# Kernel tuning notes

Hardware: AMD Instinct MI355X
Metric: run time of the kernel (lower is better)

## Reference

```python
import jax, jax.numpy as jnp
import numpy as np

B = 16384
QD = 2048   # query_dim
KD = 1024   # key_dim
HID = 1024  # hidden_dim = min(QD, KD)
NH = 16     # num_heads
HD = HID // NH  # head_dim = 64
LN_EPS = 1e-5


def _ln(x, w, b):
    m = jnp.mean(x, axis=-1, keepdims=True)
    v = jnp.mean((x - m) ** 2, axis=-1, keepdims=True)
    return (x - m) * jax.lax.rsqrt(v + LN_EPS) * w + b


def _lin(x, W, b):
    return x @ W.T + b


def setup_inputs() -> dict:
    key = jax.random.key(0)
    ks = jax.random.split(key, 12)
    p = lambda k, shape: jax.random.normal(k, shape, jnp.float32) * 0.02
    return dict(
        query_features=jax.random.normal(ks[0], (B, QD), jnp.float32),
        key_features=jax.random.normal(ks[1], (B, KD), jnp.float32),
        Wq=p(ks[2], (HID, QD)), bq=jnp.zeros((HID,), jnp.float32),
        ln_q_w=jnp.ones((HID,), jnp.float32), ln_q_b=jnp.zeros((HID,), jnp.float32),
        Wk=p(ks[3], (HID, KD)), bk=jnp.zeros((HID,), jnp.float32),
        ln_k_w=jnp.ones((HID,), jnp.float32), ln_k_b=jnp.zeros((HID,), jnp.float32),
        Wvq=p(ks[4], (HID, QD)), bvq=jnp.zeros((HID,), jnp.float32),
        Wvk=p(ks[5], (HID, KD)), bvk=jnp.zeros((HID,), jnp.float32),
        Wo=p(ks[6], (QD, HID)), bo=jnp.zeros((QD,), jnp.float32),
        ln_o_w=jnp.ones((QD,), jnp.float32), ln_o_b=jnp.zeros((QD,), jnp.float32),
        Wg1=p(ks[7], (HID, QD + KD)), bg1=jnp.zeros((HID,), jnp.float32),
        Wg2=p(ks[8], (1, HID)), bg2=jnp.zeros((1,), jnp.float32),
        Wc1=p(ks[9], (HID, QD + KD)), bc1=jnp.zeros((HID,), jnp.float32),
        Wc2=p(ks[10], (1, HID)), bc2=jnp.zeros((1,), jnp.float32),
    )


def reference(query_features, key_features,
              Wq, bq, ln_q_w, ln_q_b,
              Wk, bk, ln_k_w, ln_k_b,
              Wvq, bvq, Wvk, bvk,
              Wo, bo, ln_o_w, ln_o_b,
              Wg1, bg1, Wg2, bg2,
              Wc1, bc1, Wc2, bc2):
    b = query_features.shape[0]
    q = _ln(_lin(query_features, Wq, bq), ln_q_w, ln_q_b)      # [B, HID]
    k = _ln(_lin(key_features, Wk, bk), ln_k_w, ln_k_b)        # [B, HID]
    v_q = _lin(query_features, Wvq, bvq)  # computed in torch but unused
    v_k = _lin(key_features, Wvk, bvk)    # [B, HID]
    q = q.reshape(b, NH, HD)
    k = k.reshape(b, NH, HD)
    v_k = v_k.reshape(b, NH, HD)
    # NOTE: attention mixes over the HEAD axis (j == num_heads), per original einsum
    scores = jnp.einsum('bhd,bjd->bhj', q, k) / np.sqrt(HD).astype(np.float32)
    attn = jax.nn.softmax(scores, axis=-1)  # dropout p effectively 0 / eval mode
    attended = jnp.einsum('bhj,bjd->bhd', attn, v_k).reshape(b, HID)
    output = _ln(_lin(attended, Wo, bo), ln_o_w, ln_o_b)       # [B, QD]
    combined = jnp.concatenate([query_features, key_features], axis=1)  # [B, QD+KD]
    gate = jax.nn.sigmoid(_lin(jax.nn.gelu(_lin(combined, Wg1, bg1), approximate=False), Wg2, bg2))
    chem = jax.nn.sigmoid(_lin(jax.nn.gelu(_lin(combined, Wc1, bc1), approximate=False), Wc2, bc2))
    effective_gate = gate * chem  # [B, 1]
    return query_features + effective_gate * output
```

## Files before the change

kernel.cpp:

```cpp
#include <hip/hip_runtime.h>
#include <stdint.h>

#define QD 2048
#define KD 1024
#define HID 1024
#define NH 16
#define HD 64
#define CMBD 3072

typedef float  f32x4   __attribute__((ext_vector_type(4)));
typedef short  short8  __attribute__((ext_vector_type(8)));
typedef short  short4v __attribute__((ext_vector_type(4)));
typedef float  float4v __attribute__((ext_vector_type(4)));

__device__ inline float bf2f(short s) {
  unsigned u = ((unsigned)(unsigned short)s) << 16;
  return __builtin_bit_cast(float, u);
}
__device__ inline short f2bf(float f) {
  unsigned u = __builtin_bit_cast(unsigned, f);
  u = u + 0x7fff + ((u >> 16) & 1);
  return (short)(u >> 16);
}

__global__ void cvt_bf16(const float* __restrict__ s, short* __restrict__ d) {
  size_t i = ((size_t)blockIdx.x * blockDim.x + threadIdx.x) * 4;
  float4v v = *(const float4v*)(s + i);
  short4v o;
  o[0] = f2bf(v[0]); o[1] = f2bf(v[1]); o[2] = f2bf(v[2]); o[3] = f2bf(v[3]);
  *(short4v*)(d + i) = o;
}

__global__ void cvt_concat(const float* __restrict__ s, short* __restrict__ d,
                           int ncols4, int ldd) {
  int i = blockIdx.x * blockDim.x + threadIdx.x;
  int row = i / ncols4;
  int c4  = i - row * ncols4;
  float4v v = *(const float4v*)(s + (size_t)row * (ncols4 * 4) + c4 * 4);
  short4v o;
  o[0] = f2bf(v[0]); o[1] = f2bf(v[1]); o[2] = f2bf(v[2]); o[3] = f2bf(v[3]);
  *(short4v*)(d + (size_t)row * ldd + c4 * 4) = o;
}

#define EPI_NONE 0
#define EPI_GELU 1

typedef const __attribute__((address_space(1))) void gvoid_t;
typedef __attribute__((address_space(3))) void lvoid_t;

#define WAIT_VM(n)  asm volatile("s_waitcnt vmcnt(" #n ")" ::: "memory")

template<int EPI>
__global__ __launch_bounds__(512, 2)
void gemm256(const short* __restrict__ A, size_t lda,
             const short* __restrict__ W,
             const float* __restrict__ bias,
             short* __restrict__ C, int N, int K) {
  extern __shared__ short ls[];
  const int tid  = threadIdx.x;
  const int lane = tid & 63;
  const int wave = tid >> 6;
  const int wm = wave >> 2, wn = wave & 3;
  const int fr = lane & 15, kq4 = lane >> 4;

  const int nwg = gridDim.x * gridDim.y;
  const int lin = blockIdx.y * gridDim.x + blockIdx.x;
  const int cpx = nwg >> 3;
  const int nid = (lin & 7) * cpx + (lin >> 3);
  const int bx = nid % gridDim.x, by = nid / gridDim.x;
  const size_t rowBase = (size_t)by * 256;
  const size_t colBase = (size_t)bx * 256;

  const int NT = K >> 5;

  f32x4 acc[8][4];
#pragma unroll
  for (int mi = 0; mi < 8; mi++)
#pragma unroll
    for (int ni = 0; ni < 4; ni++) acc[mi][ni] = (f32x4){0.f, 0.f, 0.f, 0.f};

  const int frsw = (kq4 ^ ((fr >> 1) & 3)) * 8;
  const int aoff = (wm * 128 + fr) * 32 + frsw;
  const int boff = 8192 + (wn * 64 + fr) * 32 + frsw;

  const int grow  = tid >> 2;
  const int slotx = (tid & 3) ^ ((tid >> 3) & 3);
  const short* pA0 = A + (rowBase + grow) * lda + slotx * 8;
  const short* pA1 = pA0 + (size_t)128 * lda;
  const short* pB0 = W + (colBase + grow) * (size_t)K + slotx * 8;
  const short* pB1 = pB0 + (size_t)128 * K;
  short* const dst0 = ls + tid * 8;

  auto STAGE = [&](int slot) {
    short* d = dst0 + slot * 16384;
    __builtin_amdgcn_global_load_lds((gvoid_t*)pA0, (lvoid_t*)d,           16, 0, 0);
    __builtin_amdgcn_global_load_lds((gvoid_t*)pA1, (lvoid_t*)(d + 4096),  16, 0, 0);
    __builtin_amdgcn_global_load_lds((gvoid_t*)pB0, (lvoid_t*)(d + 8192),  16, 0, 0);
    __builtin_amdgcn_global_load_lds((gvoid_t*)pB1, (lvoid_t*)(d + 12288), 16, 0, 0);
    pA0 += 32; pA1 += 32; pB0 += 32; pB1 += 32;
  };

  STAGE(0); STAGE(1); STAGE(2);
  WAIT_VM(4);
  __builtin_amdgcn_s_barrier();

  short8 cf[12], nf[12];
  {
    const short* sl = ls;
#pragma unroll
    for (int m = 0; m < 8; m++) cf[m] = *(const short8*)(sl + aoff + m * 512);
#pragma unroll
    for (int n = 0; n < 4; n++) cf[8 + n] = *(const short8*)(sl + boff + n * 512);
  }

  for (int i = 0; i < NT; i += 2) {
    {
      if (i + 3 < NT) STAGE((i + 3) & 3);
      const short* sl = ls + ((i + 1) & 3) * 16384;
#pragma unroll
      for (int m = 0; m < 8; m++) nf[m] = *(const short8*)(sl + aoff + m * 512);
#pragma unroll
      for (int n = 0; n < 4; n++) nf[8 + n] = *(const short8*)(sl + boff + n * 512);
      __builtin_amdgcn_s_setprio(1);
#pragma unroll
      for (int m = 0; m < 8; m++)
#pragma unroll
        for (int n = 0; n < 4; n++)
          acc[m][n] = __builtin_amdgcn_mfma_f32_16x16x32_bf16(cf[m], cf[8 + n], acc[m][n], 0, 0, 0);
      __builtin_amdgcn_s_setprio(0);
      if (i + 3 < NT) { WAIT_VM(4); } else { WAIT_VM(0); }
      __builtin_amdgcn_s_barrier();
    }
    {
      if (i + 4 < NT) STAGE((i + 4) & 3);
      if (i + 2 < NT) {
        const short* sl = ls + ((i + 2) & 3) * 16384;
#pragma unroll
        for (int m = 0; m < 8; m++) cf[m] = *(const short8*)(sl + aoff + m * 512);
#pragma unroll
        for (int n = 0; n < 4; n++) cf[8 + n] = *(const short8*)(sl + boff + n * 512);
      }
      __builtin_amdgcn_s_setprio(1);
#pragma unroll
      for (int m = 0; m < 8; m++)
#pragma unroll
        for (int n = 0; n < 4; n++)
          acc[m][n] = __builtin_amdgcn_mfma_f32_16x16x32_bf16(nf[m], nf[8 + n], acc[m][n], 0, 0, 0);
      __builtin_amdgcn_s_setprio(0);
      if (i + 4 < NT) { WAIT_VM(4); } else { WAIT_VM(0); }
      __builtin_amdgcn_s_barrier();
    }
  }

#pragma unroll
  for (int mi = 0; mi < 8; mi++) {
    const size_t row0 = rowBase + wm * 128 + mi * 16 + kq4 * 4;
#pragma unroll
    for (int ni = 0; ni < 4; ni++) {
      const int col = (int)colBase + wn * 64 + ni * 16 + fr;
      const float bv = bias[col];
#pragma unroll
      for (int j = 0; j < 4; j++) {
        float x = acc[mi][ni][j] + bv;
        if (EPI == EPI_GELU) x = 0.5f * x * (1.f + erff(x * 0.70710678118f));
        C[(row0 + j) * (size_t)N + col] = f2bf(x);
      }
    }
  }
}

__device__ inline float2 block_sum2(float a, float b, float* sc) {
#pragma unroll
  for (int o = 32; o >= 1; o >>= 1) {
    a += __shfl_down(a, o);
    b += __shfl_down(b, o);
  }
  const int lane = threadIdx.x & 63, w = threadIdx.x >> 6;
  const int nw = blockDim.x >> 6;
  if (lane == 0) { sc[w * 2] = a; sc[w * 2 + 1] = b; }
  __syncthreads();
  float ra = 0.f, rb = 0.f;
  for (int i = 0; i < nw; i++) { ra += sc[i * 2]; rb += sc[i * 2 + 1]; }
  __syncthreads();
  return make_float2(ra, rb);
}

__global__ __launch_bounds__(256)
void attn_ln(const short* __restrict__ qp, const short* __restrict__ kv,
             const float* __restrict__ lnqw, const float* __restrict__ lnqb,
             const float* __restrict__ lnkw, const float* __restrict__ lnkb,
             short* __restrict__ att) {
  __shared__ float qs[HID];
  __shared__ float ks[NH * 65];
  __shared__ float vs[HID];
  __shared__ float aw[256];
  __shared__ float red[8];
  const int t = threadIdx.x;
  const size_t row = blockIdx.x;

  short4v q4 = *(const short4v*)(qp + row * HID + t * 4);
  short4v k4 = *(const short4v*)(kv + row * 2048 + t * 4);
  short4v v4 = *(const short4v*)(kv + row * 2048 + 1024 + t * 4);
  float qv[4], kvv[4];
  float sq = 0.f, sqq = 0.f, sk = 0.f, skk = 0.f;
#pragma unroll
  for (int i = 0; i < 4; i++) {
    qv[i] = bf2f(q4[i]); sq += qv[i]; sqq += qv[i] * qv[i];
    kvv[i] = bf2f(k4[i]); sk += kvv[i]; skk += kvv[i] * kvv[i];
  }
  float2 rq = block_sum2(sq, sqq, red);
  float mq = rq.x / HID, vq = rq.y / HID - mq * mq;
  float rsq = rsqrtf(vq + 1e-5f);
  float2 rk = block_sum2(sk, skk, red);
  float mk = rk.x / HID, vv = rk.y / HID - mk * mk;
  float rsk = rsqrtf(vv + 1e-5f);
#pragma unroll
  for (int i = 0; i < 4; i++) {
    const int idx = t * 4 + i;
    qs[idx] = (qv[i] - mq) * rsq * lnqw[idx] + lnqb[idx];
    ks[(idx >> 6) * 65 + (idx & 63)] = (kvv[i] - mk) * rsk * lnkw[idx] + lnkb[idx];
    vs[idx] = bf2f(v4[i]);
  }
  __syncthreads();

  const int h = t >> 4, j = t & 15;
  float s = 0.f;
#pragma unroll 8
  for (int d = 0; d < 64; d++) s += qs[h * 64 + d] * ks[j * 65 + d];
  s *= 0.125f;
  float mx = s;
#pragma unroll
  for (int o = 8; o >= 1; o >>= 1) mx = fmaxf(mx, __shfl_xor(mx, o, 16));
  float e = __expf(s - mx);
  float sum = e;
#pragma unroll
  for (int o = 8; o >= 1; o >>= 1) sum += __shfl_xor(sum, o, 16);
  aw[t] = e / sum;
  __syncthreads();

  const int dB = (t & 15) * 4;
  float o0 = 0.f, o1 = 0.f, o2 = 0.f, o3 = 0.f;
#pragma unroll
  for (int jj = 0; jj < 16; jj++) {
    const float w = aw[h * 16 + jj];
    const float* vp = &vs[jj * 64 + dB];
    o0 += w * vp[0]; o1 += w * vp[1]; o2 += w * vp[2]; o3 += w * vp[3];
  }
  short4v o4;
  o4[0] = f2bf(o0); o4[1] = f2bf(o1); o4[2] = f2bf(o2); o4[3] = f2bf(o3);
  *(short4v*)(att + row * HID + h * 64 + dB) = o4;
}

__global__ __launch_bounds__(256)
void gate_kernel(const short* __restrict__ hgc,
                 const float* __restrict__ wg2, const float* __restrict__ bg2,
                 const float* __restrict__ wc2, const float* __restrict__ bc2,
                 float* __restrict__ eg) {
  __shared__ float red[8];
  const int t = threadIdx.x;
  const size_t row = blockIdx.x;
  short4v g4 = *(const short4v*)(hgc + row * 2048 + t * 4);
  short4v c4 = *(const short4v*)(hgc + row * 2048 + 1024 + t * 4);
  float sg = 0.f, sc = 0.f;
#pragma unroll
  for (int i = 0; i < 4; i++) {
    sg += bf2f(g4[i]) * wg2[t * 4 + i];
    sc += bf2f(c4[i]) * wc2[t * 4 + i];
  }
  float2 r = block_sum2(sg, sc, red);
  if (t == 0) {
    float g = 1.f / (1.f + __expf(-(r.x + bg2[0])));
    float c = 1.f / (1.f + __expf(-(r.y + bc2[0])));
    eg[row] = g * c;
  }
}

__global__ __launch_bounds__(256)
void final_kernel(const short* __restrict__ opre, const float* __restrict__ qf,
                  const float* __restrict__ eg,
                  const float* __restrict__ lnow, const float* __restrict__ lnob,
                  float* __restrict__ out) {
  __shared__ float red[8];
  const int t = threadIdx.x;
  const size_t row = blockIdx.x;
  short8 o8 = *(const short8*)(opre + row * QD + t * 8);
  float x[8];
  float s = 0.f, ss = 0.f;
#pragma unroll
  for (int i = 0; i < 8; i++) { x[i] = bf2f(o8[i]); s += x[i]; ss += x[i] * x[i]; }
  float2 r = block_sum2(s, ss, red);
  float m = r.x / QD, v = r.y / QD - m * m;
  float rs = rsqrtf(v + 1e-5f);
  float g = eg[row];
  float4v oa, ob;
#pragma unroll
  for (int i = 0; i < 8; i++) {
    const int c = t * 8 + i;
    float y = (x[i] - m) * rs * lnow[c] + lnob[c];
    float r2 = qf[row * QD + c] + g * y;
    if (i < 4) oa[i] = r2; else ob[i - 4] = r2;
  }
  *(float4v*)(out + row * QD + t * 8) = oa;
  *(float4v*)(out + row * QD + t * 8 + 4) = ob;
}

extern "C" void kernel_launch(void* const* d_in, const int* in_sizes, int n_in,
                              void* d_out, int out_size, void* d_ws, size_t ws_size,
                              hipStream_t stream) {
  const float* qf   = (const float*)d_in[0];
  const float* kf   = (const float*)d_in[1];
  const float* Wq   = (const float*)d_in[2];
  const float* bq   = (const float*)d_in[3];
  const float* lnqw = (const float*)d_in[4];
  const float* lnqb = (const float*)d_in[5];
  const float* Wk   = (const float*)d_in[6];
  const float* bk   = (const float*)d_in[7];
  const float* lnkw = (const float*)d_in[8];
  const float* lnkb = (const float*)d_in[9];
  const float* Wvk  = (const float*)d_in[12];
  const float* bvk  = (const float*)d_in[13];
  const float* Wo   = (const float*)d_in[14];
  const float* bo   = (const float*)d_in[15];
  const float* lnow = (const float*)d_in[16];
  const float* lnob = (const float*)d_in[17];
  const float* Wg1  = (const float*)d_in[18];
  const float* bg1  = (const float*)d_in[19];
  const float* Wg2  = (const float*)d_in[20];
  const float* bg2  = (const float*)d_in[21];
  const float* Wc1  = (const float*)d_in[22];
  const float* bc1  = (const float*)d_in[23];
  const float* Wc2  = (const float*)d_in[24];
  const float* bc2  = (const float*)d_in[25];

  const int rows = in_sizes[0] / QD;

  char* ws = (char*)d_ws;
  size_t off = 0;
  auto alloc = [&](size_t bytes) -> char* {
    char* p = ws + off;
    off += (bytes + 255) & ~(size_t)255;
    return p;
  };
  short* cmb  = (short*)alloc((size_t)rows * CMBD * 2);
  short* wqb  = (short*)alloc((size_t)HID * QD * 2);
  short* wkv  = (short*)alloc((size_t)2 * HID * KD * 2);
  short* wob  = (short*)alloc((size_t)QD * HID * 2);
  short* wgc  = (short*)alloc((size_t)2 * HID * CMBD * 2);
  short* hgc  = (short*)alloc((size_t)rows * 2048 * 2);
  short* qp   = (short*)alloc((size_t)rows * HID * 2);
  short* kvp  = (short*)alloc((size_t)rows * 2048 * 2);
  float* eg   = (float*)alloc((size_t)rows * 4);
  float* bgc  = (float*)alloc(2048 * 4);
  float* bkv  = (float*)alloc(2048 * 4);
  short* att  = hgc;
  short* opre = cmb;

  hipMemcpyAsync(bgc, bg1, HID * 4, hipMemcpyDeviceToDevice, stream);
  hipMemcpyAsync(bgc + HID, bc1, HID * 4, hipMemcpyDeviceToDevice, stream);
  hipMemcpyAsync(bkv, bk, HID * 4, hipMemcpyDeviceToDevice, stream);
  hipMemcpyAsync(bkv + HID, bvk, HID * 4, hipMemcpyDeviceToDevice, stream);

  cvt_concat<<<rows * 2, 256, 0, stream>>>(qf, cmb, QD / 4, CMBD);
  cvt_concat<<<rows, 256, 0, stream>>>(kf, cmb + QD, KD / 4, CMBD);
  cvt_bf16<<<(HID * QD / 4) / 256, 256, 0, stream>>>(Wq, wqb);
  cvt_bf16<<<(HID * KD / 4) / 256, 256, 0, stream>>>(Wk, wkv);
  cvt_bf16<<<(HID * KD / 4) / 256, 256, 0, stream>>>(Wvk, wkv + (size_t)HID * KD);
  cvt_bf16<<<(QD * HID / 4) / 256, 256, 0, stream>>>(Wo, wob);
  cvt_bf16<<<(HID * CMBD / 4) / 256, 256, 0, stream>>>(Wg1, wgc);
  cvt_bf16<<<(HID * CMBD / 4) / 256, 256, 0, stream>>>(Wc1, wgc + (size_t)HID * CMBD);

  hipFuncSetAttribute((const void*)gemm256<EPI_GELU>,
                      hipFuncAttributeMaxDynamicSharedMemorySize, 131072);
  hipFuncSetAttribute((const void*)gemm256<EPI_NONE>,
                      hipFuncAttributeMaxDynamicSharedMemorySize, 131072);

  const dim3 blk(512);
  const int mt = rows / 256;
  const size_t lds = 131072;

  gemm256<EPI_GELU><<<dim3(2048 / 256, mt), blk, lds, stream>>>(cmb, CMBD, wgc, bgc, hgc, 2048, CMBD);
  gate_kernel<<<rows, 256, 0, stream>>>(hgc, Wg2, bg2, Wc2, bc2, eg);
  gemm256<EPI_NONE><<<dim3(1024 / 256, mt), blk, lds, stream>>>(cmb, CMBD, wqb, bq, qp, 1024, QD);
  gemm256<EPI_NONE><<<dim3(2048 / 256, mt), blk, lds, stream>>>(cmb + QD, CMBD, wkv, bkv, kvp, 2048, KD);
  attn_ln<<<rows, 256, 0, stream>>>(qp, kvp, lnqw, lnqb, lnkw, lnkb, att);
  gemm256<EPI_NONE><<<dim3(2048 / 256, mt), blk, lds, stream>>>(att, HID, wob, bo, opre, 2048, HID);
  final_kernel<<<rows, 256, 0, stream>>>(opre, qf, eg, lnow, lnob, (float*)d_out);
}
```

Before: 651.8 us.

## Restructure GEMM mainloop into eight-phase ping-pong with split A/B panel staging

Replaces the four-slot, one-tile-per-stage pipeline in the bf16 MFMA GEMM with a two-buffer scheme that steps K in 64-wide tiles. Each tile is split into quadrant phases, and every phase issues a single A or B half-panel prefetch. Fragment LDS reads and MFMA quadrants are interleaved with barriers and lgkmcnt waits. The goal is to spread global-to-LDS traffic evenly and hide LDS read latency behind MFMA work, at the cost of many more barriers per K step and more intricate buffer-hazard ordering.

```diff
diff --git a/kernel.cpp b/kernel.cpp
--- a/kernel.cpp
+++ b/kernel.cpp
@@ -49,6 +49,18 @@
 typedef __attribute__((address_space(3))) void lvoid_t;
 
 #define WAIT_VM(n)  asm volatile("s_waitcnt vmcnt(" #n ")" ::: "memory")
+
+#define APAN(b, kp) (((b) * 2 + (kp)) * 8192)
+#define BPAN(b, kp) (32768 + ((b) * 2 + (kp)) * 8192)
+
+#define PHASE_MID                                        \
+  __builtin_amdgcn_s_barrier();                          \
+  asm volatile("s_waitcnt lgkmcnt(0)" ::: "memory");     \
+  __builtin_amdgcn_s_setprio(1);
+
+#define PHASE_END                                        \
+  __builtin_amdgcn_s_setprio(0);                         \
+  __builtin_amdgcn_s_barrier();
 
 template<int EPI>
 __global__ __launch_bounds__(512, 2)
@@ -71,7 +83,7 @@
   const size_t rowBase = (size_t)by * 256;
   const size_t colBase = (size_t)bx * 256;
 
-  const int NT = K >> 5;
+  const int NTT = K >> 6;
 
   f32x4 acc[8][4];
 #pragma unroll
@@ -80,76 +92,177 @@
     for (int ni = 0; ni < 4; ni++) acc[mi][ni] = (f32x4){0.f, 0.f, 0.f, 0.f};
 
   const int frsw = (kq4 ^ ((fr >> 1) & 3)) * 8;
-  const int aoff = (wm * 128 + fr) * 32 + frsw;
-  const int boff = 8192 + (wn * 64 + fr) * 32 + frsw;
 
   const int grow  = tid >> 2;
   const int slotx = (tid & 3) ^ ((tid >> 3) & 3);
-  const short* pA0 = A + (rowBase + grow) * lda + slotx * 8;
-  const short* pA1 = pA0 + (size_t)128 * lda;
-  const short* pB0 = W + (colBase + grow) * (size_t)K + slotx * 8;
-  const short* pB1 = pB0 + (size_t)128 * K;
-  short* const dst0 = ls + tid * 8;
-
-  auto STAGE = [&](int slot) {
-    short* d = dst0 + slot * 16384;
-    __builtin_amdgcn_global_load_lds((gvoid_t*)pA0, (lvoid_t*)d,           16, 0, 0);
-    __builtin_amdgcn_global_load_lds((gvoid_t*)pA1, (lvoid_t*)(d + 4096),  16, 0, 0);
-    __builtin_amdgcn_global_load_lds((gvoid_t*)pB0, (lvoid_t*)(d + 8192),  16, 0, 0);
-    __builtin_amdgcn_global_load_lds((gvoid_t*)pB1, (lvoid_t*)(d + 12288), 16, 0, 0);
-    pA0 += 32; pA1 += 32; pB0 += 32; pB1 += 32;
+  const short* gAlo = A + (rowBase + grow) * lda + slotx * 8;
+  const short* gAhi = gAlo + (size_t)128 * lda;
+  const short* gBlo = W + (colBase + grow) * (size_t)K + slotx * 8;
+  const short* gBhi = gBlo + (size_t)128 * K;
+  short* const sdst = ls + tid * 8;
+
+  auto STG_A = [&](int panOff, int kcol) {
+    __builtin_amdgcn_global_load_lds((gvoid_t*)(gAlo + kcol), (lvoid_t*)(sdst + panOff),        16, 0, 0);
+    __builtin_amdgcn_global_load_lds((gvoid_t*)(gAhi + kcol), (lvoid_t*)(sdst + panOff + 4096), 16, 0, 0);
   };
-
-  STAGE(0); STAGE(1); STAGE(2);
+  auto STG_B = [&](int panOff, int kcol) {
+    __builtin_amdgcn_global_load_lds((gvoid_t*)(gBlo + kcol), (lvoid_t*)(sdst + panOff),        16, 0, 0);
+    __builtin_amdgcn_global_load_lds((gvoid_t*)(gBhi + kcol), (lvoid_t*)(sdst + panOff + 4096), 16, 0, 0);
+  };
+
+  STG_A(APAN(0, 0), 0);  STG_A(APAN(0, 1), 32);
+  STG_B(BPAN(0, 0), 0);  STG_B(BPAN(0, 1), 32);
+  STG_B(BPAN(1, 0), 64); STG_B(BPAN(1, 1), 96);
   WAIT_VM(4);
   __builtin_amdgcn_s_barrier();
 
-  short8 cf[12], nf[12];
-  {
-    const short* sl = ls;
-#pragma unroll
-    for (int m = 0; m < 8; m++) cf[m] = *(const short8*)(sl + aoff + m * 512);
-#pragma unroll
-    for (int n = 0; n < 4; n++) cf[8 + n] = *(const short8*)(sl + boff + n * 512);
-  }
-
-  for (int i = 0; i < NT; i += 2) {
-    {
-      if (i + 3 < NT) STAGE((i + 3) & 3);
-      const short* sl = ls + ((i + 1) & 3) * 16384;
-#pragma unroll
-      for (int m = 0; m < 8; m++) nf[m] = *(const short8*)(sl + aoff + m * 512);
-#pragma unroll
-      for (int n = 0; n < 4; n++) nf[8 + n] = *(const short8*)(sl + boff + n * 512);
-      __builtin_amdgcn_s_setprio(1);
-#pragma unroll
-      for (int m = 0; m < 8; m++)
-#pragma unroll
-        for (int n = 0; n < 4; n++)
-          acc[m][n] = __builtin_amdgcn_mfma_f32_16x16x32_bf16(cf[m], cf[8 + n], acc[m][n], 0, 0, 0);
-      __builtin_amdgcn_s_setprio(0);
-      if (i + 3 < NT) { WAIT_VM(4); } else { WAIT_VM(0); }
-      __builtin_amdgcn_s_barrier();
-    }
-    {
-      if (i + 4 < NT) STAGE((i + 4) & 3);
-      if (i + 2 < NT) {
-        const short* sl = ls + ((i + 2) & 3) * 16384;
-#pragma unroll
-        for (int m = 0; m < 8; m++) cf[m] = *(const short8*)(sl + aoff + m * 512);
-#pragma unroll
-        for (int n = 0; n < 4; n++) cf[8 + n] = *(const short8*)(sl + boff + n * 512);
-      }
-      __builtin_amdgcn_s_setprio(1);
-#pragma unroll
-      for (int m = 0; m < 8; m++)
-#pragma unroll
-        for (int n = 0; n < 4; n++)
-          acc[m][n] = __builtin_amdgcn_mfma_f32_16x16x32_bf16(nf[m], nf[8 + n], acc[m][n], 0, 0, 0);
-      __builtin_amdgcn_s_setprio(0);
-      if (i + 4 < NT) { WAIT_VM(4); } else { WAIT_VM(0); }
-      __builtin_amdgcn_s_barrier();
-    }
+  short8 fa0[8], fa1[8], fb0[4], fb1[4];
+
+  for (int t = 0; t < NTT; t += 2) {
+    const bool more = (t + 2 < NTT);
+    const int kA1 = (t + 1) * 64;
+    const int kE2 = (t + 2) * 64;
+    const int kO3 = (t + 3) * 64;
+
+#pragma unroll
+    for (int m = 0; m < 4; m++) {
+      const int r = (wm * 128 + m * 16 + fr) * 32 + frsw;
+      fa0[m * 2 + 0] = *(const short8*)(ls + APAN(0, 0) + r);
+      fa0[m * 2 + 1] = *(const short8*)(ls + APAN(0, 1) + r);
+    }
+#pragma unroll
+    for (int n = 0; n < 2; n++) {
+      const int r = (wn * 64 + n * 16 + fr) * 32 + frsw;
+      fb0[n * 2 + 0] = *(const short8*)(ls + BPAN(0, 0) + r);
+      fb0[n * 2 + 1] = *(const short8*)(ls + BPAN(0, 1) + r);
+    }
+    STG_A(APAN(1, 0), kA1);
+    PHASE_MID
+#pragma unroll
+    for (int m = 0; m < 4; m++)
+#pragma unroll
+      for (int n = 0; n < 2; n++) {
+        acc[m][n] = __builtin_amdgcn_mfma_f32_16x16x32_bf16(fa0[m*2+0], fb0[n*2+0], acc[m][n], 0, 0, 0);
+        acc[m][n] = __builtin_amdgcn_mfma_f32_16x16x32_bf16(fa0[m*2+1], fb0[n*2+1], acc[m][n], 0, 0, 0);
+      }
+    PHASE_END
+
+#pragma unroll
+    for (int n = 0; n < 2; n++) {
+      const int r = (wn * 64 + (n + 2) * 16 + fr) * 32 + frsw;
+      fb1[n * 2 + 0] = *(const short8*)(ls + BPAN(0, 0) + r);
+      fb1[n * 2 + 1] = *(const short8*)(ls + BPAN(0, 1) + r);
+    }
+    STG_A(APAN(1, 1), kA1 + 32);
+    PHASE_MID
+#pragma unroll
+    for (int m = 0; m < 4; m++)
+#pragma unroll
+      for (int n = 0; n < 2; n++) {
+        acc[m][n+2] = __builtin_amdgcn_mfma_f32_16x16x32_bf16(fa0[m*2+0], fb1[n*2+0], acc[m][n+2], 0, 0, 0);
+        acc[m][n+2] = __builtin_amdgcn_mfma_f32_16x16x32_bf16(fa0[m*2+1], fb1[n*2+1], acc[m][n+2], 0, 0, 0);
+      }
+    PHASE_END
+
+#pragma unroll
+    for (int m = 0; m < 4; m++) {
+      const int r = (wm * 128 + (m + 4) * 16 + fr) * 32 + frsw;
+      fa1[m * 2 + 0] = *(const short8*)(ls + APAN(0, 0) + r);
+      fa1[m * 2 + 1] = *(const short8*)(ls + APAN(0, 1) + r);
+    }
+    if (more) STG_B(BPAN(0, 0), kE2);
+    PHASE_MID
+#pragma unroll
+    for (int m = 0; m < 4; m++)
+#pragma unroll
+      for (int n = 0; n < 2; n++) {
+        acc[m+4][n] = __builtin_amdgcn_mfma_f32_16x16x32_bf16(fa1[m*2+0], fb0[n*2+0], acc[m+4][n], 0, 0, 0);
+        acc[m+4][n] = __builtin_amdgcn_mfma_f32_16x16x32_bf16(fa1[m*2+1], fb0[n*2+1], acc[m+4][n], 0, 0, 0);
+      }
+    PHASE_END
+
+    if (more) STG_B(BPAN(0, 1), kE2 + 32);
+    PHASE_MID
+#pragma unroll
+    for (int m = 0; m < 4; m++)
+#pragma unroll
+      for (int n = 0; n < 2; n++) {
+        acc[m+4][n+2] = __builtin_amdgcn_mfma_f32_16x16x32_bf16(fa1[m*2+0], fb1[n*2+0], acc[m+4][n+2], 0, 0, 0);
+        acc[m+4][n+2] = __builtin_amdgcn_mfma_f32_16x16x32_bf16(fa1[m*2+1], fb1[n*2+1], acc[m+4][n+2], 0, 0, 0);
+      }
+    __builtin_amdgcn_s_setprio(0);
+    if (more) { WAIT_VM(4); } else { WAIT_VM(0); }
+    __builtin_amdgcn_s_barrier();
+
+#pragma unroll
+    for (int m = 0; m < 4; m++) {
+      const int r = (wm * 128 + m * 16 + fr) * 32 + frsw;
+      fa0[m * 2 + 0] = *(const short8*)(ls + APAN(1, 0) + r);
+      fa0[m * 2 + 1] = *(const short8*)(ls + APAN(1, 1) + r);
+    }
+#pragma unroll
+    for (int n = 0; n < 2; n++) {
+      const int r = (wn * 64 + n * 16 + fr) * 32 + frsw;
+      fb0[n * 2 + 0] = *(const short8*)(ls + BPAN(1, 0) + r);
+      fb0[n * 2 + 1] = *(const short8*)(ls + BPAN(1, 1) + r);
+    }
+    if (more) STG_A(APAN(0, 0), kE2);
+    PHASE_MID
+#pragma unroll
+    for (int m = 0; m < 4; m++)
+#pragma unroll
+      for (int n = 0; n < 2; n++) {
+        acc[m][n] = __builtin_amdgcn_mfma_f32_16x16x32_bf16(fa0[m*2+0], fb0[n*2+0], acc[m][n], 0, 0, 0);
+        acc[m][n] = __builtin_amdgcn_mfma_f32_16x16x32_bf16(fa0[m*2+1], fb0[n*2+1], acc[m][n], 0, 0, 0);
+      }
+    PHASE_END
+
+#pragma unroll
+    for (int n = 0; n < 2; n++) {
+      const int r = (wn * 64 + (n + 2) * 16 + fr) * 32 + frsw;
+      fb1[n * 2 + 0] = *(const short8*)(ls + BPAN(1, 0) + r);
+      fb1[n * 2 + 1] = *(const short8*)(ls + BPAN(1, 1) + r);
+    }
+    if (more) STG_A(APAN(0, 1), kE2 + 32);
+    PHASE_MID
+#pragma unroll
+    for (int m = 0; m < 4; m++)
+#pragma unroll
+      for (int n = 0; n < 2; n++) {
+        acc[m][n+2] = __builtin_amdgcn_mfma_f32_16x16x32_bf16(fa0[m*2+0], fb1[n*2+0], acc[m][n+2], 0, 0, 0);
+        acc[m][n+2] = __builtin_amdgcn_mfma_f32_16x16x32_bf16(fa0[m*2+1], fb1[n*2+1], acc[m][n+2], 0, 0, 0);
+      }
+    PHASE_END
+
+#pragma unroll
+    for (int m = 0; m < 4; m++) {
+      const int r = (wm * 128 + (m + 4) * 16 + fr) * 32 + frsw;
+      fa1[m * 2 + 0] = *(const short8*)(ls + APAN(1, 0) + r);
+      fa1[m * 2 + 1] = *(const short8*)(ls + APAN(1, 1) + r);
+    }
+    if (more) STG_B(BPAN(1, 0), kO3);
+    PHASE_MID
+#pragma unroll
+    for (int m = 0; m < 4; m++)
+#pragma unroll
+      for (int n = 0; n < 2; n++) {
+        acc[m+4][n] = __builtin_amdgcn_mfma_f32_16x16x32_bf16(fa1[m*2+0], fb0[n*2+0], acc[m+4][n], 0, 0, 0);
+        acc[m+4][n] = __builtin_amdgcn_mfma_f32_16x16x32_bf16(fa1[m*2+1], fb0[n*2+1], acc[m+4][n], 0, 0, 0);
+      }
+    PHASE_END
+
+    if (more) STG_B(BPAN(1, 1), kO3 + 32);
+    PHASE_MID
+#pragma unroll
+    for (int m = 0; m < 4; m++)
+#pragma unroll
+      for (int n = 0; n < 2; n++) {
+        acc[m+4][n+2] = __builtin_amdgcn_mfma_f32_16x16x32_bf16(fa1[m*2+0], fb1[n*2+0], acc[m+4][n+2], 0, 0, 0);
+        acc[m+4][n+2] = __builtin_amdgcn_mfma_f32_16x16x32_bf16(fa1[m*2+1], fb1[n*2+1], acc[m+4][n+2], 0, 0, 0);
+      }
+    __builtin_amdgcn_s_setprio(0);
+    if (more) { WAIT_VM(4); }
+    __builtin_amdgcn_s_barrier();
   }
 
 #pragma unroll
```

Measured after the change: 634.4 us. 1.03x faster.
